# Performance work log

Hardware: AMD Instinct MI355X
Metric: run time of the kernel (lower is better)

The kernel has to match this reference:

```python
import jax, jax.numpy as jnp
import numpy as np

NUM_VIEWS = 24
SLOPE = 0.2
P = 14 * 14  # 196 spatial features per view
OUT = 1024


def setup_inputs() -> dict:
    key = jax.random.key(0)
    ks = jax.random.split(key, 6)
    B = 16384
    x = jax.random.normal(ks[0], (B, 14, 14, NUM_VIEWS), dtype=jnp.float32)
    indices = jax.random.randint(ks[1], (NUM_VIEWS,), 0, NUM_VIEWS, dtype=jnp.int64)
    # fc_idx: Linear(num_views -> 196); fc_aggre: Linear(392 -> 1024)
    W_idx = jax.random.normal(ks[2], (P, NUM_VIEWS), dtype=jnp.float32) * (1.0 / np.sqrt(NUM_VIEWS))
    b_idx = jax.random.normal(ks[3], (P,), dtype=jnp.float32) * 0.01
    W_aggre = jax.random.normal(ks[4], (OUT, 2 * P), dtype=jnp.float32) * (1.0 / np.sqrt(2 * P))
    b_aggre = jax.random.normal(ks[5], (OUT,), dtype=jnp.float32) * 0.01
    return {"x": x, "indices": indices, "W_idx": W_idx, "b_idx": b_idx,
            "W_aggre": W_aggre, "b_aggre": b_aggre}


def reference(x, indices, W_idx, b_idx, W_aggre, b_aggre):
    B, s1, s2, s3 = x.shape
    K = indices.shape[0]
    xr = x.reshape(B, s1 * s2, s3)            # [B, 196, V]
    # one-hot index path is batch-independent: compute once per idx
    oh = jax.nn.one_hot(indices, s3, dtype=x.dtype)                # [K, V]
    infer_index = jax.nn.leaky_relu(oh @ W_idx.T + b_idx, SLOPE)   # [K, 196]
    x_sel = jnp.take(xr, indices, axis=2)                          # [B, 196, K]
    # fc_aggre(cat(x_part, idx_part)) summed over K, split weight by halves
    Wx = W_aggre[:, :s1 * s2]   # [1024, 196] acts on x part
    Wi = W_aggre[:, s1 * s2:]   # [1024, 196] acts on index part
    out_x = jnp.einsum('bpk,op->bo', x_sel, Wx)                    # [B, 1024]
    out_i = infer_index.sum(axis=0) @ Wi.T                         # [1024]
    out = out_x + out_i + K * b_aggre                              # broadcast over batch
    return out
```

## Files before the change

kernel.cpp:

```cpp
#include <hip/hip_runtime.h>

#define B_ROWS 16384
#define PDIM 196
#define KPAD 224
#define NV 24
#define OUT_DIM 1024
#define SLOPE 0.2f

typedef __attribute__((ext_vector_type(8))) short short8;
typedef __attribute__((ext_vector_type(4))) float floatx4;

static __device__ __forceinline__ unsigned short f2bf(float f) {
    union { float f; unsigned int u; } v; v.f = f;
    unsigned int r = v.u + 0x7fffu + ((v.u >> 16) & 1u);
    return (unsigned short)(r >> 16);
}

__global__ __launch_bounds__(256) void prep_k(
        const int* __restrict__ idx,
        const float* __restrict__ W_idx,
        const float* __restrict__ b_idx,
        const float* __restrict__ W_aggre,
        const float* __restrict__ b_aggre,
        unsigned short* __restrict__ Bp,
        float* __restrict__ cvec) {
    int t = threadIdx.x;
    if (blockIdx.x < 112) {
        int tid = blockIdx.x * 256 + t;
        int ks = tid >> 12;
        int rem = tid & 4095;
        int nt = rem >> 6;
        int lane = rem & 63;
        int n = nt * 16 + (lane & 15);
        int kb = ks * 32 + (lane >> 4) * 8;
        unsigned short* dst = Bp + (size_t)tid * 8;
        #pragma unroll
        for (int j = 0; j < 8; ++j) {
            int k = kb + j;
            float v = (k < PDIM) ? W_aggre[(size_t)n * (2 * PDIM) + k] : 0.f;
            dst[j] = f2bf(v);
        }
    } else {
        __shared__ float v_sh[PDIM];
        __shared__ int idx_sh[NV];
        if (t < NV) idx_sh[t] = idx[t];
        __syncthreads();
        if (t < PDIM) {
            float bp = b_idx[t];
            float a = 0.f;
            #pragma unroll
            for (int k = 0; k < NV; ++k) {
                float z = W_idx[t * NV + idx_sh[k]] + bp;
                a += (z > 0.f) ? z : SLOPE * z;
            }
            v_sh[t] = a;
        }
        __syncthreads();
        int bc = blockIdx.x - 112;
        int o = bc * 32 + (t >> 3);
        int pl = t & 7;
        const float* wr = W_aggre + (size_t)o * (2 * PDIM) + PDIM;
        float a = 0.f;
        for (int p = pl; p < PDIM; p += 8) a += v_sh[p] * wr[p];
        a += __shfl_down(a, 4, 8);
        a += __shfl_down(a, 2, 8);
        a += __shfl_down(a, 1, 8);
        if (pl == 0) cvec[o] = a + (float)NV * b_aggre[o];
    }
}

static __device__ __forceinline__ void stage_tile(
        const float* __restrict__ x, const float* scnt,
        unsigned short* sbuf, int rowbase, int t) {
    #pragma unroll 4
    for (int i = 0; i < 14; ++i) {
        int sl = t + 256 * i;
        unsigned row16 = (unsigned)sl / 224u;
        unsigned p = (unsigned)sl - row16 * 224u;
        float a = 0.f;
        if (p < PDIM) {
            const float4* x4 = (const float4*)(x + ((size_t)(rowbase + row16) * PDIM + p) * NV);
            #pragma unroll
            for (int q = 0; q < 6; ++q) {
                float4 v = x4[q];
                a += scnt[4 * q + 0] * v.x + scnt[4 * q + 1] * v.y +
                     scnt[4 * q + 2] * v.z + scnt[4 * q + 3] * v.w;
            }
        }
        unsigned ks = p >> 5, qd = (p >> 3) & 3, j = p & 7;
        sbuf[(ks * 64 + qd * 16 + row16) * 8 + j] = (p < PDIM) ? f2bf(a) : (unsigned short)0;
    }
}

static __device__ __forceinline__ void gemm_tile(
        const unsigned short* sbuf, const unsigned short* __restrict__ Bp,
        const float* __restrict__ cvec, float* __restrict__ out,
        int rowbase, int t) {
    int lane = t & 63, wave = t >> 6;
    int quad = lane >> 4, l15 = lane & 15;

    short8 af[7];
    #pragma unroll
    for (int ks = 0; ks < 7; ++ks)
        af[ks] = *(const short8*)(sbuf + (ks * 64 + lane) * 8);

    floatx4 acc[16];
    #pragma unroll
    for (int nt = 0; nt < 16; ++nt) acc[nt] = (floatx4){0.f, 0.f, 0.f, 0.f};

    const unsigned short* bbase = Bp + ((size_t)(wave * 16) * 64 + lane) * 8;
    #pragma unroll
    for (int ks = 0; ks < 7; ++ks) {
        #pragma unroll
        for (int nt = 0; nt < 16; ++nt) {
            short8 bf = *(const short8*)(bbase + (size_t)(ks * 64 + nt) * 64 * 8);
            acc[nt] = __builtin_amdgcn_mfma_f32_16x16x32_bf16(af[ks], bf, acc[nt], 0, 0, 0);
        }
    }

    int row0 = rowbase + quad * 4;
    float* orow = out + (size_t)row0 * OUT_DIM + wave * 256 + l15;
    #pragma unroll
    for (int nt = 0; nt < 16; ++nt) {
        float cv = cvec[wave * 256 + nt * 16 + l15];
        float* po = orow + nt * 16;
        po[0 * OUT_DIM] = acc[nt][0] + cv;
        po[1 * OUT_DIM] = acc[nt][1] + cv;
        po[2 * OUT_DIM] = acc[nt][2] + cv;
        po[3 * OUT_DIM] = acc[nt][3] + cv;
    }
}

__global__ __launch_bounds__(256) void fused_k(
        const float* __restrict__ x,
        const int* __restrict__ idx,
        const unsigned short* __restrict__ Bp,
        const float* __restrict__ cvec,
        float* __restrict__ out) {
    __shared__ float scnt[NV];
    __shared__ unsigned short sA[2][7 * 64 * 8] __attribute__((aligned(16)));
    int t = threadIdx.x;

    if (t < NV) {
        int c = 0;
        #pragma unroll
        for (int k = 0; k < NV; ++k) c += (idx[k] == t);
        scnt[t] = (float)c;
    }
    __syncthreads();

    int rb0 = blockIdx.x * 32;

    stage_tile(x, scnt, sA[0], rb0, t);
    __syncthreads();

    stage_tile(x, scnt, sA[1], rb0 + 16, t);
    gemm_tile(sA[0], Bp, cvec, out, rb0, t);
    __syncthreads();

    gemm_tile(sA[1], Bp, cvec, out, rb0 + 16, t);
}

extern "C" void kernel_launch(void* const* d_in, const int* in_sizes, int n_in,
                              void* d_out, int out_size, void* d_ws, size_t ws_size,
                              hipStream_t stream) {
    const float* x       = (const float*)d_in[0];
    const int*   idx     = (const int*)d_in[1];
    const float* W_idx   = (const float*)d_in[2];
    const float* b_idx   = (const float*)d_in[3];
    const float* W_aggre = (const float*)d_in[4];
    const float* b_aggre = (const float*)d_in[5];
    float* out = (float*)d_out;

    char* ws = (char*)d_ws;
    float*          cvec = (float*)ws;
    unsigned short* Bp   = (unsigned short*)(ws + 4096);

    hipLaunchKernelGGL(prep_k, dim3(144), dim3(256), 0, stream,
                       idx, W_idx, b_idx, W_aggre, b_aggre, Bp, cvec);
    hipLaunchKernelGGL(fused_k, dim3(B_ROWS / 32), dim3(256), 0, stream,
                       x, idx, Bp, cvec, out);
}
```

Measured before the change: 464.2 us.

## Interleave second tile's x staging with first tile's MFMA loop

Replaces the sequential stage-then-gemm of the first half tile with a manually interleaved loop. Each k-step issues the B fragment loads and the global x loads for two staging slots, runs the 16 MFMAs, then reduces the x values into the second LDS buffer. The goal is to hide global load latency behind matrix math inside a wave, not only across waves. This raises register pressure (16 B fragments plus 12 float4 per thread), which may lower occupancy.

```diff
diff --git a/kernel.cpp b/kernel.cpp
--- a/kernel.cpp
+++ b/kernel.cpp
@@ -113,7 +113,7 @@
     for (int ks = 0; ks < 7; ++ks) {
         #pragma unroll
         for (int nt = 0; nt < 16; ++nt) {
-            short8 bf = *(const short8*)(bbase + (size_t)(ks * 64 + nt) * 64 * 8);
+            short8 bf = *(const short8*)(bbase + (size_t)(ks * 64 + nt) * 512);
             acc[nt] = __builtin_amdgcn_mfma_f32_16x16x32_bf16(af[ks], bf, acc[nt], 0, 0, 0);
         }
     }
@@ -154,8 +154,73 @@
     stage_tile(x, scnt, sA[0], rb0, t);
     __syncthreads();
 
-    stage_tile(x, scnt, sA[1], rb0 + 16, t);
-    gemm_tile(sA[0], Bp, cvec, out, rb0, t);
+    {
+        int lane = t & 63, wave = t >> 6;
+        int quad = lane >> 4, l15 = lane & 15;
+
+        short8 af[7];
+        #pragma unroll
+        for (int ks = 0; ks < 7; ++ks)
+            af[ks] = *(const short8*)(sA[0] + (ks * 64 + lane) * 8);
+
+        floatx4 acc[16];
+        #pragma unroll
+        for (int nt = 0; nt < 16; ++nt) acc[nt] = (floatx4){0.f, 0.f, 0.f, 0.f};
+
+        const unsigned short* bbase = Bp + ((size_t)(wave * 16) * 64 + lane) * 8;
+
+        #pragma unroll
+        for (int ks = 0; ks < 7; ++ks) {
+            short8 bf[16];
+            #pragma unroll
+            for (int nt = 0; nt < 16; ++nt)
+                bf[nt] = *(const short8*)(bbase + (size_t)(ks * 64 + nt) * 512);
+            float4 r[2][6];
+            unsigned pp[2], rw[2];
+            #pragma unroll
+            for (int u = 0; u < 2; ++u) {
+                int sl = t + 256 * (2 * ks + u);
+                unsigned row16 = (unsigned)sl / 224u;
+                unsigned p = (unsigned)sl - row16 * 224u;
+                rw[u] = row16; pp[u] = p;
+                if (p < PDIM) {
+                    const float4* x4 = (const float4*)(x + ((size_t)(rb0 + 16 + row16) * PDIM + p) * NV);
+                    #pragma unroll
+                    for (int q = 0; q < 6; ++q) r[u][q] = x4[q];
+                }
+            }
+            #pragma unroll
+            for (int nt = 0; nt < 16; ++nt)
+                acc[nt] = __builtin_amdgcn_mfma_f32_16x16x32_bf16(af[ks], bf[nt], acc[nt], 0, 0, 0);
+            #pragma unroll
+            for (int u = 0; u < 2; ++u) {
+                float a = 0.f;
+                if (pp[u] < PDIM) {
+                    #pragma unroll
+                    for (int q = 0; q < 6; ++q) {
+                        float4 v = r[u][q];
+                        a += scnt[4 * q + 0] * v.x + scnt[4 * q + 1] * v.y +
+                             scnt[4 * q + 2] * v.z + scnt[4 * q + 3] * v.w;
+                    }
+                }
+                unsigned k2 = pp[u] >> 5, qd = (pp[u] >> 3) & 3, j = pp[u] & 7;
+                sA[1][(k2 * 64 + qd * 16 + rw[u]) * 8 + j] =
+                    (pp[u] < PDIM) ? f2bf(a) : (unsigned short)0;
+            }
+        }
+
+        int row0 = rb0 + quad * 4;
+        float* orow = out + (size_t)row0 * OUT_DIM + wave * 256 + l15;
+        #pragma unroll
+        for (int nt = 0; nt < 16; ++nt) {
+            float cv = cvec[wave * 256 + nt * 16 + l15];
+            float* po = orow + nt * 16;
+            po[0 * OUT_DIM] = acc[nt][0] + cv;
+            po[1 * OUT_DIM] = acc[nt][1] + cv;
+            po[2 * OUT_DIM] = acc[nt][2] + cv;
+            po[3 * OUT_DIM] = acc[nt][3] + cv;
+        }
+    }
     __syncthreads();
 
     gemm_tile(sA[1], Bp, cvec, out, rb0 + 16, t);
```

After: 459.8 us. Within noise of the previous version (-0.9%).
